# Kernel optimization log

Hardware: AMD Instinct MI355X
Metric: run time of the kernel (lower is better)

## Reference

```python
import jax, jax.numpy as jnp
import numpy as np

P_DIM = 128
NV = 33000; NP_ = 33000; ND = 33000
N = NV + NP_ + ND            # 99000 nodes
E = 800000                    # edges
G = 64                        # graphs in batch
R = 4                         # message-passing iterations


def setup_inputs() -> dict:
    key = jax.random.key(0)
    ks = jax.random.split(key, 24)
    f = lambda k, s: jax.random.normal(k, s, dtype=jnp.float32)
    w = lambda k, s: 0.05 * jax.random.normal(k, s, dtype=jnp.float32)
    inp = {
        "edge_attr": f(ks[0], (E,)),
        "node_mu": f(ks[1], (N, P_DIM)),
        "x_vehicle": f(ks[2], (NV, 2)),
        "x_pickup": f(ks[3], (NP_, 3)),
        "x_dropoff": f(ks[4], (ND, 2)),
        # torch Linear weights stored as (in, out); y = x @ W + b
        "W1": w(ks[5], (P_DIM, P_DIM)), "b1": w(ks[6], (P_DIM,)),
        "W2": w(ks[7], (P_DIM, P_DIM)), "b2": w(ks[8], (P_DIM,)),
        "W3": w(ks[9], (1, P_DIM)),     "b3": w(ks[10], (P_DIM,)),
        "Wv": w(ks[11], (2, P_DIM)),    "bv": w(ks[12], (P_DIM,)),
        "Wp": w(ks[13], (3, P_DIM)),    "bp": w(ks[14], (P_DIM,)),
        "Wd": w(ks[15], (2, P_DIM)),    "bd": w(ks[16], (P_DIM,)),
        "Wc": w(ks[17], (P_DIM, 1)),    "bc": w(ks[18], (1,)),
        "edge_index": jax.random.randint(ks[19], (2, E), 0, N),
        # block layout: first NV vehicles (type 0), then pickups (1), dropoffs (2)
        "node_types": jnp.concatenate([
            jnp.zeros((NV,), jnp.int32),
            jnp.ones((NP_,), jnp.int32),
            jnp.full((ND,), 2, jnp.int32)]),
        "batch": jnp.sort(jax.random.randint(ks[20], (N,), 0, G)),
        "num_graphs": G,
    }
    return inp


def reference(edge_attr, node_mu, x_vehicle, x_pickup, x_dropoff,
              W1, b1, W2, b2, W3, b3, Wv, bv, Wp, bp, Wd, bd, Wc, bc,
              edge_index, node_types, batch, num_graphs):
    n_nodes = node_mu.shape[0]
    src, dst = edge_index[0], edge_index[1]

    # theta3 on edge attrs (constant across iterations -> hoisted, same math)
    t = jax.nn.leaky_relu(edge_attr[:, None] @ W3 + b3)          # (E, p)
    agg_t = jax.ops.segment_sum(t, dst, num_segments=n_nodes)    # (N, p)
    t_term = agg_t @ W2 + b2                                     # theta2 term

    # per-node-type additive transform; node types are laid out in blocks so
    # mu[mask] += Linear_t(x_t) is a block-ordered concat (constant per iter)
    type_add = jnp.concatenate([
        x_vehicle @ Wv + bv,
        x_pickup @ Wp + bp,
        x_dropoff @ Wd + bd], axis=0)                            # (N, p)

    mu = node_mu
    for _ in range(R):
        agg_mu = jax.ops.segment_sum(mu[src], dst, num_segments=n_nodes)
        mu = jax.nn.leaky_relu(agg_mu @ W1 + b1 + t_term + type_add)

    # scatter_mean over graph ids
    g_sum = jax.ops.segment_sum(mu, batch, num_segments=num_graphs)
    counts = jax.ops.segment_sum(jnp.ones((n_nodes,), mu.dtype), batch,
                                 num_segments=num_graphs)
    g = g_sum / jnp.maximum(counts, 1.0)[:, None]                # (G, p)
    proba = jax.nn.sigmoid(g @ Wc + bc)                          # (G, 1)
    return proba
```

## Files before the change

### kernel.cpp

```cpp
#include <hip/hip_runtime.h>
#include <math.h>

#define P 128

typedef __attribute__((ext_vector_type(8))) short short8;
typedef __attribute__((ext_vector_type(4))) float f32x4;

static __device__ __forceinline__ float lrelu(float x){ return x > 0.f ? x : 0.01f*x; }
static __device__ __forceinline__ float bflo(unsigned u){ union{unsigned u; float f;} c; c.u = u << 16; return c.f; }
static __device__ __forceinline__ float bfhi(unsigned u){ union{unsigned u; float f;} c; c.u = u & 0xffff0000u; return c.f; }
static __device__ __forceinline__ unsigned fbits(float f){ union{float f; unsigned u;} c; c.f = f; return c.u; }
static __device__ __forceinline__ unsigned packbf(float x, float y){
  unsigned ux = fbits(x); ux += 0x7fffu + ((ux >> 16) & 1u);
  unsigned uy = fbits(y); uy += 0x7fffu + ((uy >> 16) & 1u);
  return (ux >> 16) | (uy & 0xffff0000u);
}

__global__ void k_hist(const int* __restrict__ dst, int E, int* __restrict__ cnt){
  int i = blockIdx.x*blockDim.x + threadIdx.x;
  int i4 = i*4;
  if(i4 + 4 <= E){
    int4 d = *(const int4*)(dst + i4);
    atomicAdd(&cnt[d.x], 1); atomicAdd(&cnt[d.y], 1);
    atomicAdd(&cnt[d.z], 1); atomicAdd(&cnt[d.w], 1);
  } else {
    for(int j = i4; j < E; ++j) atomicAdd(&cnt[dst[j]], 1);
  }
}

__global__ void k_scan1(const int* __restrict__ cnt, int N, int* __restrict__ off, int* __restrict__ partial){
  __shared__ int s[256];
  int t = threadIdx.x, i = blockIdx.x*256 + t;
  int v = (i < N) ? cnt[i] : 0;
  s[t] = v; __syncthreads();
  for(int o = 1; o < 256; o <<= 1){
    int x = (t >= o) ? s[t-o] : 0; __syncthreads();
    s[t] += x; __syncthreads();
  }
  if(i < N) off[i] = s[t];
  if(t == 255) partial[blockIdx.x] = s[255];
}

__global__ void k_scan2(int* __restrict__ partial, int nb){
  __shared__ int s[512];
  int t = threadIdx.x;
  int v = (t < nb) ? partial[t] : 0;
  s[t] = v; __syncthreads();
  for(int o = 1; o < 512; o <<= 1){
    int x = (t >= o) ? s[t-o] : 0; __syncthreads();
    s[t] += x; __syncthreads();
  }
  if(t < nb) partial[t] = s[t] - v;
}

__global__ void k_scan3(const int* __restrict__ cnt, int N, int E, int* __restrict__ off, const int* __restrict__ partial){
  int i = blockIdx.x*256 + threadIdx.x;
  if(i < N) off[i] = off[i] - cnt[i] + partial[blockIdx.x];
  if(i == 0) off[N] = E;
}

__global__ void k_scatter(const int* __restrict__ ei, const float* __restrict__ ea, int E,
                          const int* __restrict__ off, int* __restrict__ cur,
                          int* __restrict__ csr_src, float* __restrict__ csr_attr){
  const int* src = ei; const int* dst = ei + E;
  int i = blockIdx.x*blockDim.x + threadIdx.x;
  int i4 = i*4;
  if(i4 + 4 <= E){
    int4   s = *(const int4*)(src + i4);
    int4   d = *(const int4*)(dst + i4);
    float4 a = *(const float4*)(ea + i4);
    int p0 = off[d.x] + atomicAdd(&cur[d.x], 1);
    int p1 = off[d.y] + atomicAdd(&cur[d.y], 1);
    int p2 = off[d.z] + atomicAdd(&cur[d.z], 1);
    int p3 = off[d.w] + atomicAdd(&cur[d.w], 1);
    csr_src[p0] = s.x; csr_attr[p0] = a.x;
    csr_src[p1] = s.y; csr_attr[p1] = a.y;
    csr_src[p2] = s.z; csr_attr[p2] = a.z;
    csr_src[p3] = s.w; csr_attr[p3] = a.w;
  } else {
    for(int j = i4; j < E; ++j){
      int d = dst[j];
      int p = off[d] + atomicAdd(&cur[d], 1);
      csr_src[p] = src[j]; csr_attr[p] = ea[j];
    }
  }
}

__global__ void k_cvt(const float2* __restrict__ in, unsigned* __restrict__ out, int n){
  int i = blockIdx.x*256 + threadIdx.x;
  if(i < n){ float2 v = in[i]; out[i] = packbf(v.x, v.y); }
}

__global__ void k_wprep(const float* __restrict__ W1, const float* __restrict__ W2,
                        unsigned* __restrict__ W1T, unsigned* __restrict__ W2T,
                        const float* __restrict__ Wv, const float* __restrict__ bv,
                        const float* __restrict__ Wp, const float* __restrict__ bp,
                        const float* __restrict__ Wd, const float* __restrict__ bd,
                        const float* __restrict__ b1, const float* __restrict__ b2,
                        unsigned* __restrict__ W2Tx){
  int b = blockIdx.x, t = threadIdx.x;
  if(b < 256){
    if(t < 64){
      const float* W = (b < 128) ? W1 : W2;
      unsigned* WT   = (b < 128) ? W1T : W2T;
      int j = b & 127, k2 = t;
      float a = W[(size_t)(2*k2)*P + j], c = W[(size_t)(2*k2+1)*P + j];
      WT[(size_t)j*64 + k2] = packbf(a, c);
    }
  } else {
    int j = t;
    unsigned q[16];
    #pragma unroll
    for(int i = 0; i < 16; ++i) q[i] = 0;
    q[0] = packbf(Wv[j],     Wv[128+j]);
    q[1] = packbf(Wp[j],     Wp[128+j]);
    q[2] = packbf(Wp[256+j], Wd[j]);
    q[3] = packbf(Wd[128+j], b1[j] + b2[j]);
    q[4] = packbf(bv[j],     bp[j]);
    q[5] = packbf(bd[j],     0.f);
    uint4* dst = (uint4*)(W2Tx + (size_t)j*16);
    #pragma unroll
    for(int i = 0; i < 4; ++i) dst[i] = make_uint4(q[4*i], q[4*i+1], q[4*i+2], q[4*i+3]);
  }
}

__global__ __launch_bounds__(512) void k_gemmB(
    const int* __restrict__ off, const float* __restrict__ csr_attr,
    const float* __restrict__ W3, const float* __restrict__ b3,
    const short8* __restrict__ WT, const short8* __restrict__ WTx,
    const float* __restrict__ xv, const float* __restrict__ xp, const float* __restrict__ xd,
    int NV, int NP_, int N, unsigned* __restrict__ Out){
  __shared__ __align__(16) unsigned shu[5376];
  __shared__ int sbound[8][9];
  int t = threadIdx.x, w = t >> 6, l = t & 63;
  int bm = blockIdx.x * 64;

  if(l < 9) sbound[w][l] = off[min(bm + w*8 + l, N)];

  {
    float w0 = W3[2*l], w1 = W3[2*l+1];
    float c0 = b3[2*l], c1 = b3[2*l+1];
    int e0 = sbound[w][0], eEnd = sbound[w][8];
    int cur = 0, nb = sbound[w][1];
    float ax = 0.f, ay = 0.f;
    auto flushTo = [&](int edge){
      while(edge >= nb){
        int row = w*8 + cur;
        shu[(row*256 + ((l*4) ^ ((row&7)<<4))) >> 2] = packbf(ax, ay);
        ax = 0.f; ay = 0.f; ++cur; nb = sbound[w][cur + 1];
      }
    };
    auto loadb = [&](float (&buf)[16], int ebase){
      #pragma unroll
      for(int k = 0; k < 16; ++k) buf[k] = csr_attr[ebase + k];
    };
    auto procb = [&](float (&buf)[16], int ebase){
      #pragma unroll
      for(int k = 0; k < 16; ++k){
        flushTo(ebase + k);
        ax += lrelu(fmaf(buf[k], w0, c0));
        ay += lrelu(fmaf(buf[k], w1, c1));
      }
    };
    int nfull = (eEnd - e0) >> 4;
    float va[16], vb[16];
    int b = 0;
    if(nfull > 0) loadb(va, e0);
    for(; b + 2 <= nfull; b += 2){
      loadb(vb, e0 + (b+1)*16);
      procb(va, e0 + b*16);
      if(b + 2 < nfull) loadb(va, e0 + (b+2)*16);
      procb(vb, e0 + (b+1)*16);
    }
    if(b < nfull) procb(va, e0 + b*16);
    int e = e0 + nfull*16;
    if(e < eEnd){
      #pragma unroll
      for(int k = 0; k < 16; ++k) va[k] = csr_attr[min(e + k, eEnd - 1)];
      #pragma unroll
      for(int k = 0; k < 16; ++k){
        if(e + k >= eEnd) break;
        flushTo(e + k);
        ax += lrelu(fmaf(va[k], w0, c0));
        ay += lrelu(fmaf(va[k], w1, c1));
      }
    }
    for(; cur < 8; ++cur){
      int row = w*8 + cur;
      shu[(row*256 + ((l*4) ^ ((row&7)<<4))) >> 2] = packbf(ax, ay);
      ax = 0.f; ay = 0.f;
    }
  }
  {
    int r = t >> 3, q = t & 7;
    int node = bm + r;
    float x0=0.f, x1=0.f, x2=0.f; int ty = 3;
    if(node < N){
      if(node < NV){ ty = 0; x0 = xv[2*node]; x1 = xv[2*node+1]; }
      else if(node < NV + NP_){ int i2 = node - NV; ty = 1; x0 = xp[3*i2]; x1 = xp[3*i2+1]; x2 = xp[3*i2+2]; }
      else { int i2 = node - NV - NP_; ty = 2; x0 = xd[2*i2]; x1 = xd[2*i2+1]; }
    }
    float s0v, s1v;
    switch(q){
      case 0: s0v = (ty==0)?x0:0.f; s1v = (ty==0)?x1:0.f; break;
      case 1: s0v = (ty==1)?x0:0.f; s1v = (ty==1)?x1:0.f; break;
      case 2: s0v = (ty==1)?x2:0.f; s1v = (ty==2)?x0:0.f; break;
      case 3: s0v = (ty==2)?x1:0.f; s1v = (node<N)?1.f:0.f; break;
      case 4: s0v = (ty==0)?1.f:0.f; s1v = (ty==1)?1.f:0.f; break;
      case 5: s0v = (ty==2)?1.f:0.f; s1v = 0.f; break;
      default: s0v = 0.f; s1v = 0.f; break;
    }
    shu[4096 + r*20 + q]     = packbf(s0v, s1v);
    shu[4096 + r*20 + 8 + q] = 0u;
  }
  __syncthreads();

  int lr = l & 15, lg = l >> 4;
  int wm = w & 3, wn = w >> 2;
  f32x4 acc[4];
  #pragma unroll
  for(int i = 0; i < 4; ++i) acc[i] = (f32x4)0.f;
  int arow = wm*16 + lr;
  #pragma unroll
  for(int ks = 0; ks < 4; ++ks){
    short8 a = *(const short8*)((const char*)shu + arow*256 + ((((ks*4+lg)*16) ^ ((arow&7)<<4))));
    #pragma unroll
    for(int ct = 0; ct < 4; ++ct){
      short8 b = WT[(size_t)(wn*64 + ct*16 + lr)*16 + ks*4 + lg];
      acc[ct] = __builtin_amdgcn_mfma_f32_16x16x32_bf16(a, b, acc[ct], 0, 0, 0);
    }
  }
  {
    short8 a = *(const short8*)&shu[4096 + arow*20 + lg*4];
    #pragma unroll
    for(int ct = 0; ct < 4; ++ct){
      short8 b = WTx[(size_t)(wn*64 + ct*16 + lr)*4 + lg];
      acc[ct] = __builtin_amdgcn_mfma_f32_16x16x32_bf16(a, b, acc[ct], 0, 0, 0);
    }
  }
  __syncthreads();

  float* shf = (float*)shu;
  int r = t >> 3, seg = t & 7;
  int row = bm + r;
  #pragma unroll
  for(int h = 0; h < 2; ++h){
    if(wn == h){
      #pragma unroll
      for(int ct = 0; ct < 4; ++ct)
        #pragma unroll
        for(int rr = 0; rr < 4; ++rr)
          shf[(wm*16 + lg*4 + rr)*68 + ct*16 + lr] = acc[ct][rr];
    }
    __syncthreads();
    if(row < N){
      float4 v0 = *(const float4*)&shf[r*68 + seg*8];
      float4 v1 = *(const float4*)&shf[r*68 + seg*8 + 4];
      *(uint4*)&Out[(size_t)row*64 + h*32 + seg*4] =
        make_uint4(packbf(v0.x,v0.y), packbf(v0.z,v0.w), packbf(v1.x,v1.y), packbf(v1.z,v1.w));
    }
    __syncthreads();
  }
}

__global__ __launch_bounds__(512) void k_fused(
    const int* __restrict__ off, const int* __restrict__ csr_src,
    const unsigned* __restrict__ mu, const short8* __restrict__ WT,
    const unsigned* __restrict__ baseB, unsigned* __restrict__ Out, int N){
  __shared__ __align__(16) float shf[64*68];
  __shared__ int sbound[8][9];
  int t = threadIdx.x, w = t >> 6, l = t & 63;
  int bm = blockIdx.x * 64;
  unsigned* Albs = (unsigned*)shf;

  if(l < 9) sbound[w][l] = off[min(bm + w*8 + l, N)];

  {
    int e0   = sbound[w][0];
    int eEnd = sbound[w][8];
    int cur = 0;
    int nb = sbound[w][1];
    float ax = 0.f, ay = 0.f;
    auto flushTo = [&](int edge){
      while(edge >= nb){
        int row = w*8 + cur;
        Albs[(row*256 + ((l*4) ^ ((row&7)<<4))) >> 2] = packbf(ax, ay);
        ax = 0.f; ay = 0.f; ++cur; nb = sbound[w][cur + 1];
      }
    };
    auto loadb = [&](unsigned (&buf)[16], int ebase){
      #pragma unroll
      for(int k = 0; k < 16; ++k){
        int idx = csr_src[ebase + k];
        buf[k] = mu[(size_t)idx*64 + l];
      }
    };
    auto procb = [&](unsigned (&buf)[16], int ebase){
      #pragma unroll
      for(int k = 0; k < 16; ++k){
        flushTo(ebase + k);
        ax += bflo(buf[k]); ay += bfhi(buf[k]);
      }
    };
    int nfull = (eEnd - e0) >> 4;
    unsigned va[16], vb[16];
    int b = 0;
    if(nfull > 0) loadb(va, e0);
    for(; b + 2 <= nfull; b += 2){
      loadb(vb, e0 + (b+1)*16);
      procb(va, e0 + b*16);
      if(b + 2 < nfull) loadb(va, e0 + (b+2)*16);
      procb(vb, e0 + (b+1)*16);
    }
    if(b < nfull) procb(va, e0 + b*16);
    int e = e0 + nfull*16;
    if(e < eEnd){
      #pragma unroll
      for(int k = 0; k < 16; ++k){
        int idx = csr_src[min(e + k, eEnd - 1)];
        va[k] = mu[(size_t)idx*64 + l];
      }
      #pragma unroll
      for(int k = 0; k < 16; ++k){
        if(e + k >= eEnd) break;
        flushTo(e + k);
        ax += bflo(va[k]); ay += bfhi(va[k]);
      }
    }
    for(; cur < 8; ++cur){
      int row = w*8 + cur;
      Albs[(row*256 + ((l*4) ^ ((row&7)<<4))) >> 2] = packbf(ax, ay);
      ax = 0.f; ay = 0.f;
    }
  }
  __syncthreads();

  int lr = l & 15, lg = l >> 4;
  int wm = w & 3, wn = w >> 2;
  f32x4 acc[4];
  #pragma unroll
  for(int i = 0; i < 4; ++i) acc[i] = (f32x4)0.f;
  int arow = wm*16 + lr;
  #pragma unroll
  for(int ks = 0; ks < 4; ++ks){
    short8 a = *(const short8*)((const char*)shf + arow*256 + ((((ks*4+lg)*16) ^ ((arow&7)<<4))));
    #pragma unroll
    for(int ct = 0; ct < 4; ++ct){
      short8 b = WT[(size_t)(wn*64 + ct*16 + lr)*16 + ks*4 + lg];
      acc[ct] = __builtin_amdgcn_mfma_f32_16x16x32_bf16(a, b, acc[ct], 0, 0, 0);
    }
  }
  __syncthreads();

  int r = t >> 3, seg = t & 7;
  int row = bm + r;
  #pragma unroll
  for(int h = 0; h < 2; ++h){
    if(wn == h){
      #pragma unroll
      for(int ct = 0; ct < 4; ++ct)
        #pragma unroll
        for(int rr = 0; rr < 4; ++rr)
          shf[(wm*16 + lg*4 + rr)*68 + ct*16 + lr] = acc[ct][rr];
    }
    __syncthreads();
    if(row < N){
      float4 v0 = *(const float4*)&shf[r*68 + seg*8];
      float4 v1 = *(const float4*)&shf[r*68 + seg*8 + 4];
      const unsigned* ad = baseB + (size_t)row*64 + h*32 + seg*4;
      unsigned b0 = ad[0], b1u = ad[1], b2u = ad[2], b3u = ad[3];
      *(uint4*)&Out[(size_t)row*64 + h*32 + seg*4] = make_uint4(
        packbf(lrelu(v0.x + bflo(b0)),  lrelu(v0.y + bfhi(b0))),
        packbf(lrelu(v0.z + bflo(b1u)), lrelu(v0.w + bfhi(b1u))),
        packbf(lrelu(v1.x + bflo(b2u)), lrelu(v1.y + bfhi(b2u))),
        packbf(lrelu(v1.z + bflo(b3u)), lrelu(v1.w + bfhi(b3u))));
    }
    __syncthreads();
  }
}

#define GSB 256
__global__ void k_gsum(const unsigned* __restrict__ mu, const int* __restrict__ batch, int N,
                       float* __restrict__ gsum){
  int c = threadIdx.x & 63, sub = threadIdx.x >> 6;
  int n0 = blockIdx.x * GSB;
  int n1 = min(n0 + GSB, N);
  float ax = 0.f, ay = 0.f; int curg = -1;
  for(int n = n0 + sub; n < n1; n += 4){
    int g = batch[n];
    if(g != curg){
      if(curg >= 0){ atomicAdd(&gsum[curg*P + 2*c], ax); atomicAdd(&gsum[curg*P + 2*c + 1], ay); }
      curg = g; ax = 0.f; ay = 0.f;
    }
    unsigned v = mu[(size_t)n*64 + c];
    ax += bflo(v); ay += bfhi(v);
  }
  if(curg >= 0){ atomicAdd(&gsum[curg*P + 2*c], ax); atomicAdd(&gsum[curg*P + 2*c + 1], ay); }
}

__global__ void k_out(const float* __restrict__ gsum, const int* __restrict__ batch, int N,
                      const float* __restrict__ Wc, const float* __restrict__ bc,
                      float* __restrict__ out){
  int g = blockIdx.x, t = threadIdx.x;
  int lo = 0, hi = N;
  while(lo < hi){ int m=(lo+hi)>>1; if(batch[m] < g) lo = m+1; else hi = m; }
  int start = lo; lo = start; hi = N;
  while(lo < hi){ int m=(lo+hi)>>1; if(batch[m] <= g) lo = m+1; else hi = m; }
  int cnt = lo - start;
  float cf = cnt < 1 ? 1.f : (float)cnt;
  __shared__ float red[128];
  red[t] = (gsum[g*P + t] / cf) * Wc[t];
  __syncthreads();
  for(int o = 64; o > 0; o >>= 1){ if(t < o) red[t] += red[t+o]; __syncthreads(); }
  if(t == 0) out[g] = 1.f/(1.f + expf(-(red[0] + bc[0])));
}

extern "C" void kernel_launch(void* const* d_in, const int* in_sizes, int n_in,
                              void* d_out, int out_size, void* d_ws, size_t ws_size,
                              hipStream_t stream){
  const float* edge_attr = (const float*)d_in[0];
  const float* node_mu   = (const float*)d_in[1];
  const float* xv = (const float*)d_in[2];
  const float* xp = (const float*)d_in[3];
  const float* xd = (const float*)d_in[4];
  const float* W1 = (const float*)d_in[5];  const float* b1 = (const float*)d_in[6];
  const float* W2 = (const float*)d_in[7];  const float* b2 = (const float*)d_in[8];
  const float* W3 = (const float*)d_in[9];  const float* b3 = (const float*)d_in[10];
  const float* Wv = (const float*)d_in[11]; const float* bv = (const float*)d_in[12];
  const float* Wp = (const float*)d_in[13]; const float* bp = (const float*)d_in[14];
  const float* Wd = (const float*)d_in[15]; const float* bd = (const float*)d_in[16];
  const float* Wc = (const float*)d_in[17]; const float* bc = (const float*)d_in[18];
  const int*   ei    = (const int*)d_in[19];
  const int*   batch = (const int*)d_in[21];
  const int E   = in_sizes[0];
  const int N   = in_sizes[1] / P;
  const int NV  = in_sizes[2] / 2;
  const int NP_ = in_sizes[3] / 3;
  const int G   = 64;
  float* out = (float*)d_out;

  char* w = (char*)d_ws; size_t o = 0;
  auto alloc = [&](size_t bytes)->void*{ size_t a = (o + 255) & ~(size_t)255; o = a + bytes; return (void*)(w + a); };
  int*      cntcur   = (int*)     alloc((size_t)2*N*4);
  int*      off      = (int*)     alloc((size_t)(N+1)*4);
  int*      partial  = (int*)     alloc(512*4);
  int*      csr_src  = (int*)     alloc((size_t)E*4);
  float*    csr_attr = (float*)   alloc((size_t)E*4);
  unsigned* mu0      = (unsigned*)alloc((size_t)N*64*4);
  unsigned* YA       = (unsigned*)alloc((size_t)N*64*4);
  unsigned* YB       = (unsigned*)alloc((size_t)N*64*4);
  unsigned* baseB    = (unsigned*)alloc((size_t)N*64*4);
  unsigned* W1T      = (unsigned*)alloc((size_t)P*64*4);
  unsigned* W2T      = (unsigned*)alloc((size_t)P*64*4);
  unsigned* W2Tx     = (unsigned*)alloc((size_t)P*16*4);
  float*    gsum     = (float*)   alloc((size_t)G*P*4);
  int* cnt = cntcur; int* cur = cntcur + N;

  hipMemsetAsync(cntcur, 0, (size_t)2*N*4, stream);
  hipMemsetAsync(gsum,   0, (size_t)G*P*4, stream);

  int nb = (N + 255) / 256;
  int ge4 = (E/4 + 255) / 256;
  k_hist   <<<ge4,  256, 0, stream>>>(ei + E, E, cnt);
  k_scan1  <<<nb,   256, 0, stream>>>(cnt, N, off, partial);
  k_scan2  <<<1,    512, 0, stream>>>(partial, nb);
  k_scan3  <<<nb,   256, 0, stream>>>(cnt, N, E, off, partial);
  k_scatter<<<ge4,  256, 0, stream>>>(ei, edge_attr, E, off, cur, csr_src, csr_attr);

  int nhalf = N*64;
  k_cvt  <<<(nhalf + 255)/256, 256, 0, stream>>>((const float2*)node_mu, mu0, nhalf);
  k_wprep<<<257, 128, 0, stream>>>(W1, W2, W1T, W2T, Wv, bv, Wp, bp, Wd, bd, b1, b2, W2Tx);

  int ggemm = (N + 63) / 64;
  k_gemmB<<<ggemm, 512, 0, stream>>>(off, csr_attr, W3, b3,
                                     (const short8*)W2T, (const short8*)W2Tx,
                                     xv, xp, xd, NV, NP_, N, baseB);

  k_fused<<<ggemm, 512, 0, stream>>>(off, csr_src, mu0, (const short8*)W1T, baseB, YA, N);
  k_fused<<<ggemm, 512, 0, stream>>>(off, csr_src, YA,  (const short8*)W1T, baseB, YB, N);
  k_fused<<<ggemm, 512, 0, stream>>>(off, csr_src, YB,  (const short8*)W1T, baseB, YA, N);
  k_fused<<<ggemm, 512, 0, stream>>>(off, csr_src, YA,  (const short8*)W1T, baseB, YB, N);

  k_gsum<<<(N + GSB - 1)/GSB, 256, 0, stream>>>(YB, batch, N, gsum);
  k_out <<<G, P, 0, stream>>>(gsum, batch, N, Wc, bc, out);
}
```

Baseline: 579.2 us.

## Interleave CSR src/attr, fold mu conversion into weight prep, drop double-buffered gathers

The separate csr_src and csr_attr arrays are merged into one int2 array, so the scatter does one 8-byte store per edge instead of two 4-byte stores. The bf16 conversion of node_mu moves into the weight-prep kernel as extra blocks, which removes one launch. The double-buffered software pipeline in the gather loops of k_gemmB and k_fused is replaced with a simpler single-buffer loop over 16 edges. The cost is that k_fused now reads 8 bytes per edge for the index, so it pulls twice the index traffic, and the gathers lose explicit load/compute overlap.

```diff
diff --git a/kernel.cpp b/kernel.cpp
--- a/kernel.cpp
+++ b/kernel.cpp
@@ -61,7 +61,7 @@
 
 __global__ void k_scatter(const int* __restrict__ ei, const float* __restrict__ ea, int E,
                           const int* __restrict__ off, int* __restrict__ cur,
-                          int* __restrict__ csr_src, float* __restrict__ csr_attr){
+                          int2* __restrict__ csr){
   const int* src = ei; const int* dst = ei + E;
   int i = blockIdx.x*blockDim.x + threadIdx.x;
   int i4 = i*4;
@@ -73,22 +73,17 @@
     int p1 = off[d.y] + atomicAdd(&cur[d.y], 1);
     int p2 = off[d.z] + atomicAdd(&cur[d.z], 1);
     int p3 = off[d.w] + atomicAdd(&cur[d.w], 1);
-    csr_src[p0] = s.x; csr_attr[p0] = a.x;
-    csr_src[p1] = s.y; csr_attr[p1] = a.y;
-    csr_src[p2] = s.z; csr_attr[p2] = a.z;
-    csr_src[p3] = s.w; csr_attr[p3] = a.w;
+    csr[p0] = make_int2(s.x, __float_as_int(a.x));
+    csr[p1] = make_int2(s.y, __float_as_int(a.y));
+    csr[p2] = make_int2(s.z, __float_as_int(a.z));
+    csr[p3] = make_int2(s.w, __float_as_int(a.w));
   } else {
     for(int j = i4; j < E; ++j){
       int d = dst[j];
       int p = off[d] + atomicAdd(&cur[d], 1);
-      csr_src[p] = src[j]; csr_attr[p] = ea[j];
-    }
-  }
-}
-
-__global__ void k_cvt(const float2* __restrict__ in, unsigned* __restrict__ out, int n){
-  int i = blockIdx.x*256 + threadIdx.x;
-  if(i < n){ float2 v = in[i]; out[i] = packbf(v.x, v.y); }
+      csr[p] = make_int2(src[j], __float_as_int(ea[j]));
+    }
+  }
 }
 
 __global__ void k_wprep(const float* __restrict__ W1, const float* __restrict__ W2,
@@ -97,7 +92,8 @@
                         const float* __restrict__ Wp, const float* __restrict__ bp,
                         const float* __restrict__ Wd, const float* __restrict__ bd,
                         const float* __restrict__ b1, const float* __restrict__ b2,
-                        unsigned* __restrict__ W2Tx){
+                        unsigned* __restrict__ W2Tx,
+                        const float4* __restrict__ mu_in, uint2* __restrict__ mu0v, int npairs){
   int b = blockIdx.x, t = threadIdx.x;
   if(b < 256){
     if(t < 64){
@@ -107,7 +103,7 @@
       float a = W[(size_t)(2*k2)*P + j], c = W[(size_t)(2*k2+1)*P + j];
       WT[(size_t)j*64 + k2] = packbf(a, c);
     }
-  } else {
+  } else if(b == 256){
     int j = t;
     unsigned q[16];
     #pragma unroll
@@ -121,11 +117,17 @@
     uint4* dst = (uint4*)(W2Tx + (size_t)j*16);
     #pragma unroll
     for(int i = 0; i < 4; ++i) dst[i] = make_uint4(q[4*i], q[4*i+1], q[4*i+2], q[4*i+3]);
+  } else {
+    int i = (b - 257)*128 + t;
+    if(i < npairs){
+      float4 v = mu_in[i];
+      mu0v[i] = make_uint2(packbf(v.x, v.y), packbf(v.z, v.w));
+    }
   }
 }
 
 __global__ __launch_bounds__(512) void k_gemmB(
-    const int* __restrict__ off, const float* __restrict__ csr_attr,
+    const int* __restrict__ off, const int2* __restrict__ csr,
     const float* __restrict__ W3, const float* __restrict__ b3,
     const short8* __restrict__ WT, const short8* __restrict__ WTx,
     const float* __restrict__ xv, const float* __restrict__ xp, const float* __restrict__ xd,
@@ -150,33 +152,22 @@
         ax = 0.f; ay = 0.f; ++cur; nb = sbound[w][cur + 1];
       }
     };
-    auto loadb = [&](float (&buf)[16], int ebase){
-      #pragma unroll
-      for(int k = 0; k < 16; ++k) buf[k] = csr_attr[ebase + k];
-    };
-    auto procb = [&](float (&buf)[16], int ebase){
-      #pragma unroll
-      for(int k = 0; k < 16; ++k){
-        flushTo(ebase + k);
-        ax += lrelu(fmaf(buf[k], w0, c0));
-        ay += lrelu(fmaf(buf[k], w1, c1));
-      }
-    };
-    int nfull = (eEnd - e0) >> 4;
-    float va[16], vb[16];
-    int b = 0;
-    if(nfull > 0) loadb(va, e0);
-    for(; b + 2 <= nfull; b += 2){
-      loadb(vb, e0 + (b+1)*16);
-      procb(va, e0 + b*16);
-      if(b + 2 < nfull) loadb(va, e0 + (b+2)*16);
-      procb(vb, e0 + (b+1)*16);
-    }
-    if(b < nfull) procb(va, e0 + b*16);
-    int e = e0 + nfull*16;
+    int e = e0;
+    for(; e + 16 <= eEnd; e += 16){
+      float va[16];
+      #pragma unroll
+      for(int k = 0; k < 16; ++k) va[k] = __int_as_float(csr[e + k].y);
+      #pragma unroll
+      for(int k = 0; k < 16; ++k){
+        flushTo(e + k);
+        ax += lrelu(fmaf(va[k], w0, c0));
+        ay += lrelu(fmaf(va[k], w1, c1));
+      }
+    }
     if(e < eEnd){
-      #pragma unroll
-      for(int k = 0; k < 16; ++k) va[k] = csr_attr[min(e + k, eEnd - 1)];
+      float va[16];
+      #pragma unroll
+      for(int k = 0; k < 16; ++k) va[k] = __int_as_float(csr[min(e + k, eEnd - 1)].y);
       #pragma unroll
       for(int k = 0; k < 16; ++k){
         if(e + k >= eEnd) break;
@@ -264,7 +255,7 @@
 }
 
 __global__ __launch_bounds__(512) void k_fused(
-    const int* __restrict__ off, const int* __restrict__ csr_src,
+    const int* __restrict__ off, const int2* __restrict__ csr,
     const unsigned* __restrict__ mu, const short8* __restrict__ WT,
     const unsigned* __restrict__ baseB, unsigned* __restrict__ Out, int N){
   __shared__ __align__(16) float shf[64*68];
@@ -288,43 +279,32 @@
         ax = 0.f; ay = 0.f; ++cur; nb = sbound[w][cur + 1];
       }
     };
-    auto loadb = [&](unsigned (&buf)[16], int ebase){
-      #pragma unroll
-      for(int k = 0; k < 16; ++k){
-        int idx = csr_src[ebase + k];
-        buf[k] = mu[(size_t)idx*64 + l];
-      }
-    };
-    auto procb = [&](unsigned (&buf)[16], int ebase){
-      #pragma unroll
-      for(int k = 0; k < 16; ++k){
-        flushTo(ebase + k);
-        ax += bflo(buf[k]); ay += bfhi(buf[k]);
-      }
-    };
-    int nfull = (eEnd - e0) >> 4;
-    unsigned va[16], vb[16];
-    int b = 0;
-    if(nfull > 0) loadb(va, e0);
-    for(; b + 2 <= nfull; b += 2){
-      loadb(vb, e0 + (b+1)*16);
-      procb(va, e0 + b*16);
-      if(b + 2 < nfull) loadb(va, e0 + (b+2)*16);
-      procb(vb, e0 + (b+1)*16);
-    }
-    if(b < nfull) procb(va, e0 + b*16);
-    int e = e0 + nfull*16;
+    int e = e0;
+    for(; e + 16 <= eEnd; e += 16){
+      unsigned v[16];
+      #pragma unroll
+      for(int k = 0; k < 16; ++k){
+        int idx = csr[e + k].x;
+        v[k] = mu[(size_t)idx*64 + l];
+      }
+      #pragma unroll
+      for(int k = 0; k < 16; ++k){
+        flushTo(e + k);
+        ax += bflo(v[k]); ay += bfhi(v[k]);
+      }
+    }
     if(e < eEnd){
-      #pragma unroll
-      for(int k = 0; k < 16; ++k){
-        int idx = csr_src[min(e + k, eEnd - 1)];
-        va[k] = mu[(size_t)idx*64 + l];
+      unsigned v[16];
+      #pragma unroll
+      for(int k = 0; k < 16; ++k){
+        int idx = csr[min(e + k, eEnd - 1)].x;
+        v[k] = mu[(size_t)idx*64 + l];
       }
       #pragma unroll
       for(int k = 0; k < 16; ++k){
         if(e + k >= eEnd) break;
         flushTo(e + k);
-        ax += bflo(va[k]); ay += bfhi(va[k]);
+        ax += bflo(v[k]); ay += bfhi(v[k]);
       }
     }
     for(; cur < 8; ++cur){
@@ -444,8 +424,7 @@
   int*      cntcur   = (int*)     alloc((size_t)2*N*4);
   int*      off      = (int*)     alloc((size_t)(N+1)*4);
   int*      partial  = (int*)     alloc(512*4);
-  int*      csr_src  = (int*)     alloc((size_t)E*4);
-  float*    csr_attr = (float*)   alloc((size_t)E*4);
+  int2*     csr      = (int2*)    alloc((size_t)E*8);
   unsigned* mu0      = (unsigned*)alloc((size_t)N*64*4);
   unsigned* YA       = (unsigned*)alloc((size_t)N*64*4);
   unsigned* YB       = (unsigned*)alloc((size_t)N*64*4);
@@ -465,21 +444,22 @@
   k_scan1  <<<nb,   256, 0, stream>>>(cnt, N, off, partial);
   k_scan2  <<<1,    512, 0, stream>>>(partial, nb);
   k_scan3  <<<nb,   256, 0, stream>>>(cnt, N, E, off, partial);
-  k_scatter<<<ge4,  256, 0, stream>>>(ei, edge_attr, E, off, cur, csr_src, csr_attr);
-
-  int nhalf = N*64;
-  k_cvt  <<<(nhalf + 255)/256, 256, 0, stream>>>((const float2*)node_mu, mu0, nhalf);
-  k_wprep<<<257, 128, 0, stream>>>(W1, W2, W1T, W2T, Wv, bv, Wp, bp, Wd, bd, b1, b2, W2Tx);
+  k_scatter<<<ge4,  256, 0, stream>>>(ei, edge_attr, E, off, cur, csr);
+
+  int npairs = N*32;
+  int gcvt = 257 + (npairs + 127)/128;
+  k_wprep<<<gcvt, 128, 0, stream>>>(W1, W2, W1T, W2T, Wv, bv, Wp, bp, Wd, bd, b1, b2, W2Tx,
+                                    (const float4*)node_mu, (uint2*)mu0, npairs);
 
   int ggemm = (N + 63) / 64;
-  k_gemmB<<<ggemm, 512, 0, stream>>>(off, csr_attr, W3, b3,
+  k_gemmB<<<ggemm, 512, 0, stream>>>(off, csr, W3, b3,
                                      (const short8*)W2T, (const short8*)W2Tx,
                                      xv, xp, xd, NV, NP_, N, baseB);
 
-  k_fused<<<ggemm, 512, 0, stream>>>(off, csr_src, mu0, (const short8*)W1T, baseB, YA, N);
-  k_fused<<<ggemm, 512, 0, stream>>>(off, csr_src, YA,  (const short8*)W1T, baseB, YB, N);
-  k_fused<<<ggemm, 512, 0, stream>>>(off, csr_src, YB,  (const short8*)W1T, baseB, YA, N);
-  k_fused<<<ggemm, 512, 0, stream>>>(off, csr_src, YA,  (const short8*)W1T, baseB, YB, N);
+  k_fused<<<ggemm, 512, 0, stream>>>(off, csr, mu0, (const short8*)W1T, baseB, YA, N);
+  k_fused<<<ggemm, 512, 0, stream>>>(off, csr, YA,  (const short8*)W1T, baseB, YB, N);
+  k_fused<<<ggemm, 512, 0, stream>>>(off, csr, YB,  (const short8*)W1T, baseB, YA, N);
+  k_fused<<<ggemm, 512, 0, stream>>>(off, csr, YA,  (const short8*)W1T, baseB, YB, N);
 
   k_gsum<<<(N + GSB - 1)/GSB, 256, 0, stream>>>(YB, batch, N, gsum);
   k_out <<<G, P, 0, stream>>>(gsum, batch, N, Wc, bc, out);
```

New measurement: 556.2 us. -4.0%, faster.
